# Kernel optimization log

Measured on AMD Instinct MI355X. Metric: run time of the kernel, lower is better.

Reference implementation:

```python
import jax, jax.numpy as jnp
import numpy as np

B, T, D, H = 64, 257, 1024, 16
F = 4096
R = 16
HD = D // H


def _layer_norm(x, g, b, eps=1e-5):
    mu = x.mean(-1, keepdims=True)
    var = x.var(-1, keepdims=True)
    return (x - mu) / jnp.sqrt(var + eps) * g + b


def _quick_gelu(x):
    return x * jax.nn.sigmoid(1.702 * x)


def _attention(x, Wq, bq, Wk, bk, Wv, bv, Wo, bo):
    scale = HD ** -0.5
    q = (x @ Wq + bq) * scale
    k = x @ Wk + bk
    v = x @ Wv + bv
    q = q.reshape(B, T, H, HD).transpose(0, 2, 1, 3)
    k = k.reshape(B, T, H, HD).transpose(0, 2, 1, 3)
    v = v.reshape(B, T, H, HD).transpose(0, 2, 1, 3)
    attn = jax.nn.softmax(jnp.einsum('bhqd,bhkd->bhqk', q, k), axis=-1)
    o = jnp.einsum('bhqk,bhkd->bhqd', attn, v)
    o = o.transpose(0, 2, 1, 3).reshape(B, T, D)
    return o @ Wo + bo


def _match_indices(metric, r, class_token=True):
    # cosine-normalized bipartite matching (no-grad path in torch; index-only here)
    m = metric / jnp.linalg.norm(metric, axis=-1, keepdims=True)
    a, b = m[:, ::2, :], m[:, 1::2, :]        # [B, ta, D], [B, tb, D]
    scores = jnp.einsum('nac,nbc->nab', a, b)  # [B, ta, tb]
    if class_token:
        scores = scores.at[:, 0, :].set(-jnp.inf)
    node_max = scores.max(-1)
    node_idx = scores.argmax(-1)
    edge_idx = jnp.argsort(-node_max, axis=-1)  # descending
    unm_idx = edge_idx[:, r:]
    src_idx = edge_idx[:, :r]
    dst_idx = jnp.take_along_axis(node_idx, src_idx, axis=-1)
    if class_token:
        unm_idx = jnp.sort(unm_idx, axis=1)
    return unm_idx, src_idx, dst_idx


def _merge_sum(x, unm_idx, src_idx, dst_idx):
    src, dst = x[:, ::2, :], x[:, 1::2, :]
    c = x.shape[-1]
    unm = jnp.take_along_axis(src, unm_idx[..., None], axis=1)       # [B, ta-r, c]
    sel = jnp.take_along_axis(src, src_idx[..., None], axis=1)       # [B, r, c]
    dst = jax.vmap(lambda d, di, sv: d.at[di].add(sv))(dst, dst_idx, sel)
    return jnp.concatenate([unm, dst], axis=1)                       # [B, T-r, c]


def setup_inputs() -> dict:
    key = jax.random.key(0)
    ks = jax.random.split(key, 12)
    s = 0.02
    return {
        'hidden_states': jax.random.normal(ks[0], (B, T, D), jnp.float32),
        'ln1_g': jnp.ones((D,), jnp.float32),
        'ln1_b': jnp.zeros((D,), jnp.float32),
        'Wq': jax.random.normal(ks[1], (D, D), jnp.float32) * s,
        'bq': jnp.zeros((D,), jnp.float32),
        'Wk': jax.random.normal(ks[2], (D, D), jnp.float32) * s,
        'bk': jnp.zeros((D,), jnp.float32),
        'Wv': jax.random.normal(ks[3], (D, D), jnp.float32) * s,
        'bv': jnp.zeros((D,), jnp.float32),
        'Wo': jax.random.normal(ks[4], (D, D), jnp.float32) * s,
        'bo': jnp.zeros((D,), jnp.float32),
        'ln2_g': jnp.ones((D,), jnp.float32),
        'ln2_b': jnp.zeros((D,), jnp.float32),
        'W1': jax.random.normal(ks[5], (D, F), jnp.float32) * s,
        'b1': jnp.zeros((F,), jnp.float32),
        'W2': jax.random.normal(ks[6], (F, D), jnp.float32) * s,
        'b2': jnp.zeros((D,), jnp.float32),
    }


def reference(hidden_states, ln1_g, ln1_b, Wq, bq, Wk, bk, Wv, bv, Wo, bo,
              ln2_g, ln2_b, W1, b1, W2, b2):
    # 1) LN1 + self-attention + residual
    x = hidden_states + _attention(_layer_norm(hidden_states, ln1_g, ln1_b),
                                   Wq, bq, Wk, bk, Wv, bv, Wo, bo)
    # 2) ToMe merge with weighted average (initial size = ones -> merge_wavg)
    metric = jax.lax.stop_gradient(x)
    unm_idx, src_idx, dst_idx = _match_indices(metric, R, class_token=True)
    size = jnp.ones((B, T, 1), x.dtype)
    x = _merge_sum(x * size, unm_idx, src_idx, dst_idx)
    size = _merge_sum(size, unm_idx, src_idx, dst_idx)
    x = x / size
    # 3) LN2 + MLP (quick_gelu) + residual
    h = _layer_norm(x, ln2_g, ln2_b)
    h = _quick_gelu(h @ W1 + b1) @ W2 + b2
    return x + h  # [B, T - R, D]
```

## Files before the change

kernel.cpp:

```cpp
#include <hip/hip_runtime.h>
#include <math.h>

#define BB 64
#define TT 257
#define DD 1024
#define HH 16
#define FF 4096
#define RR 16
#define HDD 64
#define TMM 241
#define M1 (BB*TT)
#define M2 (BB*TMM)
#define NA 129
#define NB 128

typedef float f4v __attribute__((ext_vector_type(4)));
typedef short s8v __attribute__((ext_vector_type(8)));
typedef short s4v __attribute__((ext_vector_type(4)));
typedef unsigned short us;

__device__ __forceinline__ us f2bf(float f){
  unsigned u = __float_as_uint(f);
  u += 0x7fffu + ((u >> 16) & 1u);
  return (us)(u >> 16);
}
__device__ __forceinline__ float bf2f(us h){
  return __uint_as_float(((unsigned)h) << 16);
}
__device__ __forceinline__ void gl16(const us* g, us* l){
  __builtin_amdgcn_global_load_lds((const __attribute__((address_space(1))) void*)g,
                                   (__attribute__((address_space(3))) void*)l, 16, 0, 0);
}

__global__ __launch_bounds__(64) void lnstats_kernel(const float* __restrict__ x,
                                                     float* __restrict__ st)
{
  int row = blockIdx.x, lane = threadIdx.x;
  const float* p = x + (size_t)row * DD;
  float s = 0.0f, sq = 0.0f;
  #pragma unroll
  for (int i = 0; i < 4; i++){
    float4 v = *(const float4*)(p + i * 256 + lane * 4);
    s  += v.x + v.y + v.z + v.w;
    sq += v.x*v.x + v.y*v.y + v.z*v.z + v.w*v.w;
  }
  #pragma unroll
  for (int m = 1; m < 64; m <<= 1){ s += __shfl_xor(s, m); sq += __shfl_xor(sq, m); }
  if (lane == 0){
    float mu  = s * (1.0f / DD);
    float var = sq * (1.0f / DD) - mu * mu;
    st[2*row]     = mu;
    st[2*row + 1] = 1.0f / sqrtf(var + 1e-5f);
  }
}

__global__ __launch_bounds__(256) void lncvt_kernel(const float* __restrict__ x,
    const float* __restrict__ st, const float* __restrict__ g,
    const float* __restrict__ b, us* __restrict__ out)
{
  int row = blockIdx.x, tid = threadIdx.x;
  float mu = st[2*row], rstd = st[2*row + 1];
  float4 xv = *(const float4*)(x + (size_t)row * DD + tid * 4);
  float4 gv = *(const float4*)(g + tid * 4);
  float4 bv = *(const float4*)(b + tid * 4);
  s4v o;
  o[0] = (short)f2bf((xv.x - mu) * rstd * gv.x + bv.x);
  o[1] = (short)f2bf((xv.y - mu) * rstd * gv.y + bv.y);
  o[2] = (short)f2bf((xv.z - mu) * rstd * gv.z + bv.z);
  o[3] = (short)f2bf((xv.w - mu) * rstd * gv.w + bv.w);
  *(s4v*)(out + (size_t)row * DD + tid * 4) = o;
}

__global__ __launch_bounds__(256) void wt_kernel(const float* __restrict__ src,
                                                 us* __restrict__ dhi,
                                                 us* __restrict__ dlo,
                                                 const float* __restrict__ gscale,
                                                 int K, int N)
{
  __shared__ float t[32][33];
  int tx = threadIdx.x, ty = threadIdx.y;
  int n0 = blockIdx.x * 32, k0 = blockIdx.y * 32;
  #pragma unroll
  for (int r = 0; r < 4; r++)
    t[ty + 8*r][tx] = src[(size_t)(k0 + ty + 8*r) * N + n0 + tx];
  __syncthreads();
  float gs = gscale ? gscale[k0 + tx] : 1.0f;
  #pragma unroll
  for (int r = 0; r < 4; r++){
    float f = t[tx][ty + 8*r] * gs;
    us hi = f2bf(f);
    size_t o = (size_t)(n0 + ty + 8*r) * K + k0 + tx;
    dhi[o] = hi;
    if (dlo) dlo[o] = f2bf(f - bf2f(hi));
  }
}

__global__ __launch_bounds__(256) void qc_kernel(const float* __restrict__ Wq,
    const float* __restrict__ Wk, const float* __restrict__ Wv,
    const float* __restrict__ g, const float* __restrict__ b,
    float* __restrict__ c1, float* __restrict__ c2)
{
  __shared__ float p1[4][64], p2[4][64];
  int n0 = blockIdx.x * 64;
  int kind = n0 >> 10, col0 = n0 & 1023;
  const float* W = (kind == 0) ? Wq : (kind == 1) ? Wk : Wv;
  int tx = threadIdx.x & 63, ty = threadIdx.x >> 6;
  float s1 = 0.0f, s2 = 0.0f;
  for (int k = ty; k < 1024; k += 4){
    float w = W[(size_t)k * 1024 + col0 + tx];
    s1 += g[k] * w;
    s2 += b[k] * w;
  }
  p1[ty][tx] = s1; p2[ty][tx] = s2;
  __syncthreads();
  if (ty == 0){
    c1[n0 + tx] = p1[0][tx] + p1[1][tx] + p1[2][tx] + p1[3][tx];
    c2[n0 + tx] = p2[0][tx] + p2[1][tx] + p2[2][tx] + p2[3][tx];
  }
}

__global__ __launch_bounds__(256) void qkv_kernel(const float* __restrict__ hidden,
    const us* __restrict__ WBh, const us* __restrict__ WBl,
    const float* __restrict__ bq, const float* __restrict__ bk, const float* __restrict__ bv,
    const float* __restrict__ lnstat, const float* __restrict__ c1, const float* __restrict__ c2,
    us* __restrict__ qhp, us* __restrict__ qlp, us* __restrict__ khp,
    us* __restrict__ klp, us* __restrict__ vhp, us* __restrict__ vlp)
{
  const int M = M1, K = DD;
  __shared__ __align__(16) us Ah[128*32];
  __shared__ __align__(16) us Bh[128*32];
  __shared__ __align__(16) us Al[128*32];
  __shared__ __align__(16) us Bl[128*32];
  int tid = threadIdx.x;
  int m0 = blockIdx.y * 128, n0 = blockIdx.x * 128;
  int lane = tid & 63, w = tid >> 6;
  int wr = w >> 1, wc = w & 1;
  int fr = lane & 15, fq = lane >> 4;
  f4v acc[4][4];
  f4v zero = {0.0f, 0.0f, 0.0f, 0.0f};
  #pragma unroll
  for (int i = 0; i < 4; i++)
    #pragma unroll
    for (int j = 0; j < 4; j++) acc[i][j] = zero;
  int sr = tid >> 2, sc4 = (tid & 3) * 8;
  int ar0 = m0 + sr;       if (ar0 >= M) ar0 = M - 1;
  int ar1 = m0 + 64 + sr;  if (ar1 >= M) ar1 = M - 1;
  int lr = lane >> 2, lc = (lane & 3) * 8;
  int gb0 = n0 + w*32 + lr;

  for (int kk = 0; kk < K; kk += 32){
    #pragma unroll
    for (int half = 0; half < 2; half++){
      int ar = half ? ar1 : ar0;
      const float* ap = hidden + (size_t)ar * K + kk + sc4;
      float4 fa = *(const float4*)(ap);
      float4 fb = *(const float4*)(ap + 4);
      float fv[8] = {fa.x, fa.y, fa.z, fa.w, fb.x, fb.y, fb.z, fb.w};
      s8v h, l;
      #pragma unroll
      for (int j = 0; j < 8; j++){
        us hi = f2bf(fv[j]);
        h[j] = (short)hi;
        l[j] = (short)f2bf(fv[j] - bf2f(hi));
      }
      int lrow = half * 64 + sr;
      *(s8v*)&Ah[lrow*32 + sc4] = h;
      *(s8v*)&Al[lrow*32 + sc4] = l;
    }
    gl16(WBh + (size_t)gb0 * K + kk + lc,        &Bh[(w*32)*32]);
    gl16(WBh + (size_t)(gb0 + 16) * K + kk + lc, &Bh[(w*32 + 16)*32]);
    gl16(WBl + (size_t)gb0 * K + kk + lc,        &Bl[(w*32)*32]);
    gl16(WBl + (size_t)(gb0 + 16) * K + kk + lc, &Bl[(w*32 + 16)*32]);
    __syncthreads();
    s8v ah[4], bh[4], al[4], bl[4];
    #pragma unroll
    for (int m = 0; m < 4; m++){
      ah[m] = *(const s8v*)&Ah[(wr*64 + m*16 + fr)*32 + fq*8];
      al[m] = *(const s8v*)&Al[(wr*64 + m*16 + fr)*32 + fq*8];
    }
    #pragma unroll
    for (int n = 0; n < 4; n++){
      bh[n] = *(const s8v*)&Bh[(wc*64 + n*16 + fr)*32 + fq*8];
      bl[n] = *(const s8v*)&Bl[(wc*64 + n*16 + fr)*32 + fq*8];
    }
    #pragma unroll
    for (int m = 0; m < 4; m++)
      #pragma unroll
      for (int n = 0; n < 4; n++){
        acc[m][n] = __builtin_amdgcn_mfma_f32_16x16x32_bf16(ah[m], bh[n], acc[m][n], 0, 0, 0);
        acc[m][n] = __builtin_amdgcn_mfma_f32_16x16x32_bf16(ah[m], bl[n], acc[m][n], 0, 0, 0);
        acc[m][n] = __builtin_amdgcn_mfma_f32_16x16x32_bf16(al[m], bh[n], acc[m][n], 0, 0, 0);
      }
    __syncthreads();
  }
  int kind = n0 >> 10;
  const float* bsel = (kind == 0) ? bq : (kind == 1) ? bk : bv;
  us* C0 = (kind == 0) ? qhp : (kind == 1) ? khp : vhp;
  us* C1 = (kind == 0) ? qlp : (kind == 1) ? klp : vlp;
  float scl = (kind == 0) ? 0.125f : 1.0f;
  #pragma unroll
  for (int m = 0; m < 4; m++){
    int grow0 = m0 + wr*64 + m*16 + fq*4;
    #pragma unroll
    for (int n = 0; n < 4; n++){
      int gcol = n0 + wc*64 + n*16 + fr;
      int lcn = gcol & 1023;
      int h2 = lcn >> 6, d2 = lcn & 63;
      float cc1 = c1[gcol], cc2 = c2[gcol] + bsel[lcn];
      #pragma unroll
      for (int i = 0; i < 4; i++){
        int grow = grow0 + i;
        if (grow < M){
          float mu = lnstat[2*grow], rstd = lnstat[2*grow + 1];
          int b2 = grow / 257;
          int t2 = grow - b2 * 257;
          size_t off2 = ((size_t)(b2*16 + h2) * 257 + t2) * 64 + d2;
          float v = (rstd * acc[m][n][i] - rstd * mu * cc1 + cc2) * scl;
          us hi = f2bf(v);
          C0[off2] = hi;
          C1[off2] = f2bf(v - bf2f(hi));
        }
      }
    }
  }
}

template<int AMODE, int SPLIT, int EPI>
__global__ __launch_bounds__(256) void gemm2_kernel(const us* __restrict__ Ahp,
    const us* __restrict__ Alp,
    const us* __restrict__ BTh, const us* __restrict__ BTl,
    const float* __restrict__ bias, const float* __restrict__ resid,
    void* __restrict__ C0, int M, int N, int K)
{
  __shared__ __align__(16) us Ah[128*32];
  __shared__ __align__(16) us Bh[128*32];
  __shared__ __align__(16) us Al[SPLIT ? 128*32 : 8];
  __shared__ __align__(16) us Bl[SPLIT ? 128*32 : 8];
  int tid = threadIdx.x;
  int m0 = blockIdx.y * 128, n0 = blockIdx.x * 128;
  int lane = tid & 63, w = tid >> 6;
  int wr = w >> 1, wc = w & 1;
  int fr = lane & 15, fq = lane >> 4;
  f4v acc[4][4];
  f4v zero = {0.0f, 0.0f, 0.0f, 0.0f};
  #pragma unroll
  for (int i = 0; i < 4; i++)
    #pragma unroll
    for (int j = 0; j < 4; j++) acc[i][j] = zero;
  int lr = lane >> 2, lc = (lane & 3) * 8;
  int ga0 = m0 + w*32 + lr;      if (ga0 >= M) ga0 = M - 1;
  int ga1 = m0 + w*32 + 16 + lr; if (ga1 >= M) ga1 = M - 1;
  int gb0 = n0 + w*32 + lr;
  int b2a = ga0 / 257, t2a = ga0 - b2a * 257;
  int b2b = ga1 / 257, t2b = ga1 - b2b * 257;

  for (int kk = 0; kk < K; kk += 32){
    if (AMODE == 1){
      gl16(Ahp + (size_t)ga0 * K + kk + lc, &Ah[(w*32)*32]);
      gl16(Ahp + (size_t)ga1 * K + kk + lc, &Ah[(w*32 + 16)*32]);
      if (SPLIT){
        gl16(Alp + (size_t)ga0 * K + kk + lc, &Al[(w*32)*32]);
        gl16(Alp + (size_t)ga1 * K + kk + lc, &Al[(w*32 + 16)*32]);
      }
    } else {
      int h2 = kk >> 6, d2 = (kk & 63) + lc;
      size_t o0 = ((size_t)(b2a*16 + h2) * 257 + t2a) * 64 + d2;
      size_t o1 = ((size_t)(b2b*16 + h2) * 257 + t2b) * 64 + d2;
      gl16(Ahp + o0, &Ah[(w*32)*32]);
      gl16(Ahp + o1, &Ah[(w*32 + 16)*32]);
      if (SPLIT){
        gl16(Alp + o0, &Al[(w*32)*32]);
        gl16(Alp + o1, &Al[(w*32 + 16)*32]);
      }
    }
    gl16(BTh + (size_t)gb0 * K + kk + lc,        &Bh[(w*32)*32]);
    gl16(BTh + (size_t)(gb0 + 16) * K + kk + lc, &Bh[(w*32 + 16)*32]);
    if (SPLIT){
      gl16(BTl + (size_t)gb0 * K + kk + lc,        &Bl[(w*32)*32]);
      gl16(BTl + (size_t)(gb0 + 16) * K + kk + lc, &Bl[(w*32 + 16)*32]);
    }
    __syncthreads();
    s8v ah[4], bh[4], al[4], bl[4];
    #pragma unroll
    for (int m = 0; m < 4; m++){
      ah[m] = *(const s8v*)&Ah[(wr*64 + m*16 + fr)*32 + fq*8];
      if (SPLIT) al[m] = *(const s8v*)&Al[(wr*64 + m*16 + fr)*32 + fq*8];
    }
    #pragma unroll
    for (int n = 0; n < 4; n++){
      bh[n] = *(const s8v*)&Bh[(wc*64 + n*16 + fr)*32 + fq*8];
      if (SPLIT) bl[n] = *(const s8v*)&Bl[(wc*64 + n*16 + fr)*32 + fq*8];
    }
    #pragma unroll
    for (int m = 0; m < 4; m++)
      #pragma unroll
      for (int n = 0; n < 4; n++){
        acc[m][n] = __builtin_amdgcn_mfma_f32_16x16x32_bf16(ah[m], bh[n], acc[m][n], 0, 0, 0);
        if (SPLIT){
          acc[m][n] = __builtin_amdgcn_mfma_f32_16x16x32_bf16(ah[m], bl[n], acc[m][n], 0, 0, 0);
          acc[m][n] = __builtin_amdgcn_mfma_f32_16x16x32_bf16(al[m], bh[n], acc[m][n], 0, 0, 0);
        }
      }
    __syncthreads();
  }
  #pragma unroll
  for (int m = 0; m < 4; m++){
    int grow0 = m0 + wr*64 + m*16 + fq*4;
    #pragma unroll
    for (int n = 0; n < 4; n++){
      int gcol = n0 + wc*64 + n*16 + fr;
      float bcol = bias[gcol];
      #pragma unroll
      for (int i = 0; i < 4; i++){
        int grow = grow0 + i;
        if (grow < M){
          float v = acc[m][n][i] + bcol;
          size_t off = (size_t)grow * N + gcol;
          if (EPI == 1){
            ((float*)C0)[off] = v + resid[off];
          } else {
            float gq = v / (1.0f + expf(-1.702f * v));
            ((us*)C0)[off] = f2bf(gq);
          }
        }
      }
    }
  }
}

__global__ __launch_bounds__(512, 1) void attn_flash_kernel(
    const us* __restrict__ Qh, const us* __restrict__ Ql,
    const us* __restrict__ Kh, const us* __restrict__ Klo,
    const us* __restrict__ Vh, const us* __restrict__ Vlo,
    us* Oh, us* Ol)
{
  __shared__ __align__(16) us Kl[257 * 128];
  __shared__ __align__(16) us Vl[64 * 640];
  int bh = blockIdx.x;
  const size_t hb = (size_t)bh * 257 * 64;
  int tid = threadIdx.x;
  int l = tid & 63, w = tid >> 6;
  int g = l >> 4, c = l & 15;
  const float NEG = -3.0e38f;

  {
    s8v z8 = {0,0,0,0,0,0,0,0};
    for (int idx = tid; idx < 64*640/8; idx += 512)
      *((s8v*)Vl + idx) = z8;
  }
  __syncthreads();
  for (int idx = tid; idx < 257*8; idx += 512){
    int tok = idx >> 3, ch = idx & 7;
    int sw = (tok & 7) << 4;
    s8v hv = *(const s8v*)(Kh  + hb + (size_t)tok * 64 + ch*8);
    s8v lv = *(const s8v*)(Klo + hb + (size_t)tok * 64 + ch*8);
    char* kr = (char*)Kl + tok * 256;
    *(s8v*)(kr + ((ch*16) ^ sw)) = hv;
    *(s8v*)(kr + 128 + ((ch*16) ^ sw)) = lv;
  }
  for (int idx = tid; idx < 257*8; idx += 512){
    int tok = idx >> 3, ch = idx & 7;
    s8v hv = *(const s8v*)(Vh  + hb + (size_t)tok * 64 + ch*8);
    s8v lv = *(const s8v*)(Vlo + hb + (size_t)tok * 64 + ch*8);
    #pragma unroll
    for (int j = 0; j < 8; j++){
      int d = ch*8 + j;
      char* vr = (char*)Vl + d * 1280;
      int off = (tok * 2) ^ (j << 4);
      *(us*)(vr + off) = (us)hv[j];
      *(us*)(vr + 640 + off) = (us)lv[j];
    }
  }
  __syncthreads();

  for (int qt = w; qt < 17; qt += 8){
    int t0 = qt * 16;
    int qr = t0 + c; if (qr > 256) qr = 256;
    const us* qp  = Qh + hb + (size_t)qr * 64 + g*8;
    const us* qp2 = Ql + hb + (size_t)qr * 64 + g*8;
    s8v qhi[2], qlo[2];
    qhi[0] = *(const s8v*)(qp);       qhi[1] = *(const s8v*)(qp + 32);
    qlo[0] = *(const s8v*)(qp2);      qlo[1] = *(const s8v*)(qp2 + 32);

    float m_run = NEG, l_run = 0.0f;
    f4v o4[4];
    #pragma unroll
    for (int dt = 0; dt < 4; dt++) o4[dt] = (f4v){0.0f, 0.0f, 0.0f, 0.0f};

    #pragma unroll 1
    for (int mck = 0; mck < 9; mck++){
      f4v a0, a1;
      {
        int t = 2*mck;
        int krow = t * 16 + c; if (krow > 256) krow = 256;
        char* kr = (char*)Kl + krow * 256;
        int sw = (krow & 7) << 4;
        s8v khi0 = *(const s8v*)(kr + ((g * 16) ^ sw));
        s8v khi1 = *(const s8v*)(kr + ((64 + g * 16) ^ sw));
        s8v klo0 = *(const s8v*)(kr + 128 + ((g * 16) ^ sw));
        s8v klo1 = *(const s8v*)(kr + 128 + ((64 + g * 16) ^ sw));
        f4v a = {0.0f, 0.0f, 0.0f, 0.0f};
        a = __builtin_amdgcn_mfma_f32_16x16x32_bf16(khi0, qhi[0], a, 0, 0, 0);
        a = __builtin_amdgcn_mfma_f32_16x16x32_bf16(khi1, qhi[1], a, 0, 0, 0);
        a = __builtin_amdgcn_mfma_f32_16x16x32_bf16(khi0, qlo[0], a, 0, 0, 0);
        a = __builtin_amdgcn_mfma_f32_16x16x32_bf16(khi1, qlo[1], a, 0, 0, 0);
        a = __builtin_amdgcn_mfma_f32_16x16x32_bf16(klo0, qhi[0], a, 0, 0, 0);
        a = __builtin_amdgcn_mfma_f32_16x16x32_bf16(klo1, qhi[1], a, 0, 0, 0);
        a0 = a;
      }
      if (mck < 8){
        int t = 2*mck + 1;
        int krow = t * 16 + c; if (krow > 256) krow = 256;
        char* kr = (char*)Kl + krow * 256;
        int sw = (krow & 7) << 4;
        s8v khi0 = *(const s8v*)(kr + ((g * 16) ^ sw));
        s8v khi1 = *(const s8v*)(kr + ((64 + g * 16) ^ sw));
        s8v klo0 = *(const s8v*)(kr + 128 + ((g * 16) ^ sw));
        s8v klo1 = *(const s8v*)(kr + 128 + ((64 + g * 16) ^ sw));
        f4v a = {0.0f, 0.0f, 0.0f, 0.0f};
        a = __builtin_amdgcn_mfma_f32_16x16x32_bf16(khi0, qhi[0], a, 0, 0, 0);
        a = __builtin_amdgcn_mfma_f32_16x16x32_bf16(khi1, qhi[1], a, 0, 0, 0);
        a = __builtin_amdgcn_mfma_f32_16x16x32_bf16(khi0, qlo[0], a, 0, 0, 0);
        a = __builtin_amdgcn_mfma_f32_16x16x32_bf16(khi1, qlo[1], a, 0, 0, 0);
        a = __builtin_amdgcn_mfma_f32_16x16x32_bf16(klo0, qhi[0], a, 0, 0, 0);
        a = __builtin_amdgcn_mfma_f32_16x16x32_bf16(klo1, qhi[1], a, 0, 0, 0);
        a1 = a;
      } else {
        a1 = (f4v){NEG, NEG, NEG, NEG};
        a0[0] = (g == 0) ? a0[0] : NEG;
        a0[1] = NEG; a0[2] = NEG; a0[3] = NEG;
      }
      float cm = fmaxf(fmaxf(fmaxf(a0[0], a0[1]), fmaxf(a0[2], a0[3])),
                       fmaxf(fmaxf(a1[0], a1[1]), fmaxf(a1[2], a1[3])));
      cm = fmaxf(cm, __shfl_xor(cm, 16));
      cm = fmaxf(cm, __shfl_xor(cm, 32));
      float m_new = fmaxf(m_run, cm);
      float scl = __expf(m_run - m_new);
      m_run = m_new;
      l_run *= scl;
      #pragma unroll
      for (int dt = 0; dt < 4; dt++){
        o4[dt][0] *= scl; o4[dt][1] *= scl; o4[dt][2] *= scl; o4[dt][3] *= scl;
      }
      float ls = 0.0f;
      unsigned Ph2[2][2], Pl2[2][2];
      #pragma unroll
      for (int k2 = 0; k2 < 2; k2++){
        float e0 = __expf(a0[2*k2] - m_new), e1 = __expf(a0[2*k2+1] - m_new);
        ls += e0 + e1;
        us h0 = f2bf(e0), h1 = f2bf(e1);
        Ph2[0][k2] = (unsigned)h0 | ((unsigned)h1 << 16);
        Pl2[0][k2] = (unsigned)f2bf(e0 - bf2f(h0)) | ((unsigned)f2bf(e1 - bf2f(h1)) << 16);
        float e2 = __expf(a1[2*k2] - m_new), e3 = __expf(a1[2*k2+1] - m_new);
        ls += e2 + e3;
        us h2 = f2bf(e2), h3 = f2bf(e3);
        Ph2[1][k2] = (unsigned)h2 | ((unsigned)h3 << 16);
        Pl2[1][k2] = (unsigned)f2bf(e2 - bf2f(h2)) | ((unsigned)f2bf(e3 - bf2f(h3)) << 16);
      }
      l_run += ls;
      s8v pbh, pbl;
      #pragma unroll
      for (int ww = 0; ww < 4; ww++){
        int srcl = (((g & 1) * 2 + (ww >> 1)) << 4) | c;
        unsigned h0 = (unsigned)__shfl((int)Ph2[0][ww & 1], srcl, 64);
        unsigned lo0 = (unsigned)__shfl((int)Pl2[0][ww & 1], srcl, 64);
        unsigned h1 = (unsigned)__shfl((int)Ph2[1][ww & 1], srcl, 64);
        unsigned lo1 = (unsigned)__shfl((int)Pl2[1][ww & 1], srcl, 64);
        ((unsigned*)&pbh)[ww] = (g >> 1) ? h1 : h0;
        ((unsigned*)&pbl)[ww] = (g >> 1) ? lo1 : lo0;
      }
      #pragma unroll
      for (int dt = 0; dt < 4; dt++){
        int d = dt * 16 + c;
        char* vr = (char*)Vl + d * 1280;
        int off = (mck * 64 + g * 16) ^ ((d & 7) << 4);
        s8v vh = *(const s8v*)(vr + off);
        s8v vlo = *(const s8v*)(vr + 640 + off);
        o4[dt] = __builtin_amdgcn_mfma_f32_16x16x32_bf16(vh, pbh, o4[dt], 0, 0, 0);
        o4[dt] = __builtin_amdgcn_mfma_f32_16x16x32_bf16(vh, pbl, o4[dt], 0, 0, 0);
        o4[dt] = __builtin_amdgcn_mfma_f32_16x16x32_bf16(vlo, pbh, o4[dt], 0, 0, 0);
      }
    }
    l_run += __shfl_xor(l_run, 16);
    l_run += __shfl_xor(l_run, 32);
    float inv = 1.0f / l_run;
    int qrow = t0 + c;
    if (qrow <= 256){
      us* oph = Oh + hb + (size_t)qrow * 64;
      us* opl = Ol + hb + (size_t)qrow * 64;
      #pragma unroll
      for (int dt = 0; dt < 4; dt++){
        s4v hv4, lv4;
        #pragma unroll
        for (int i = 0; i < 4; i++){
          float ov = o4[dt][i] * inv;
          us hi = f2bf(ov);
          hv4[i] = (short)hi;
          lv4[i] = (short)f2bf(ov - bf2f(hi));
        }
        *(s4v*)(oph + dt*16 + g*4) = hv4;
        *(s4v*)(opl + dt*16 + g*4) = lv4;
      }
    }
  }
}

__global__ __launch_bounds__(64) void norms_kernel(const float* __restrict__ x, float* __restrict__ nrm)
{
  int row = blockIdx.x, lane = threadIdx.x;
  const float* p = x + (size_t)row * DD;
  float sq = 0.0f;
  #pragma unroll
  for (int i = 0; i < 4; i++){
    float4 v = *(const float4*)(p + i * 256 + lane * 4);
    sq += v.x*v.x + v.y*v.y + v.z*v.z + v.w*v.w;
  }
  #pragma unroll
  for (int m = 1; m < 64; m <<= 1) sq += __shfl_xor(sq, m);
  if (lane == 0) nrm[row] = sqrtf(sq);
}

__global__ __launch_bounds__(256) void scores_kernel(const float* __restrict__ x,
                                                     const float* __restrict__ nrm,
                                                     float* __restrict__ sc)
{
  __shared__ __align__(16) float as_[16][1028];
  __shared__ __align__(16) float bs_[16][1028];
  int it = blockIdx.x, b = blockIdx.y;
  int tid = threadIdx.x;
  int rloc = tid >> 4, chunk = tid & 15;
  {
    int i = it * 16 + rloc;
    int tg = (i < NA) ? 2 * i : 2 * (NA - 1);
    const float* p = x + ((size_t)b * TT + tg) * DD + chunk * 64;
    #pragma unroll
    for (int ii = 0; ii < 16; ii++)
      *(float4*)&as_[rloc][chunk * 64 + 4*ii] = *(const float4*)(p + 4*ii);
  }
  for (int jt = 0; jt < 8; jt++){
    __syncthreads();
    {
      int j = jt * 16 + rloc;
      const float* p = x + ((size_t)b * TT + 2*j + 1) * DD + chunk * 64;
      #pragma unroll
      for (int ii = 0; ii < 16; ii++)
        *(float4*)&bs_[rloc][chunk * 64 + 4*ii] = *(const float4*)(p + 4*ii);
    }
    __syncthreads();
    int iloc = tid >> 4, jloc = tid & 15;
    float sum = 0.0f;
    #pragma unroll 8
    for (int cgg = 0; cgg < 1024; cgg += 4){
      float4 av = *(const float4*)&as_[iloc][cgg];
      float4 bvv = *(const float4*)&bs_[jloc][cgg];
      sum += av.x*bvv.x + av.y*bvv.y + av.z*bvv.z + av.w*bvv.w;
    }
    int i = it * 16 + iloc, j = jt * 16 + jloc;
    if (i < NA){
      float val = sum / (nrm[(size_t)b * TT + 2*i] * nrm[(size_t)b * TT + 2*j + 1]);
      sc[((size_t)b * NA + i) * NB + j] = val;
    }
  }
}

__global__ __launch_bounds__(64) void node_kernel(const float* __restrict__ sc,
                                                  float* __restrict__ nmax, int* __restrict__ nidx)
{
  int i = blockIdx.x, b = blockIdx.y, lane = threadIdx.x;
  const float* row = sc + ((size_t)b * NA + i) * NB;
  float v0 = row[lane];
  float v1 = row[lane + 64];
  float bv = v0; int bi = lane;
  if (v1 > bv){ bv = v1; bi = lane + 64; }
  #pragma unroll
  for (int m = 1; m < 64; m <<= 1){
    float ov = __shfl_xor(bv, m);
    int oi = __shfl_xor(bi, m);
    if (ov > bv || (ov == bv && oi < bi)){ bv = ov; bi = oi; }
  }
  if (lane == 0){
    if (i == 0){ nmax[(size_t)b * NA] = -INFINITY; nidx[(size_t)b * NA] = 0; }
    else { nmax[(size_t)b * NA + i] = bv; nidx[(size_t)b * NA + i] = bi; }
  }
}

__global__ __launch_bounds__(256) void rank_kernel(const float* __restrict__ nmax,
    const int* __restrict__ nidx, int* __restrict__ src, int* __restrict__ dst,
    int* __restrict__ unm, int* __restrict__ cnt)
{
  __shared__ float v[NA];
  __shared__ int rk[NA];
  __shared__ int edge[NA];
  __shared__ int cs[NB];
  int b = blockIdx.x, t = threadIdx.x;
  if (t < NA) v[t] = nmax[(size_t)b * NA + t];
  if (t < NB) cs[t] = 0;
  __syncthreads();
  if (t < NA){
    float vt = v[t]; int r = 0;
    for (int i = 0; i < NA; i++){
      float vi = v[i];
      r += (vi > vt) || (vi == vt && i < t);
    }
    rk[t] = r; edge[r] = t;
  }
  __syncthreads();
  if (t < RR){
    int s = edge[t];
    src[b * RR + t] = s;
    int d = nidx[(size_t)b * NA + s];
    dst[b * RR + t] = d;
    atomicAdd(&cs[d], 1);
  }
  if (t < NA && rk[t] >= RR){
    int p = 0;
    for (int i = 0; i < NA; i++) p += (i < t) && (rk[i] >= RR);
    unm[b * (NA - RR) + p] = t;
  }
  __syncthreads();
  if (t < NB) cnt[b * NB + t] = cs[t];
}

__global__ __launch_bounds__(256) void merge_kernel(const float* __restrict__ x,
    const int* __restrict__ src, const int* __restrict__ dst, const int* __restrict__ unm,
    const int* __restrict__ cnt, float* __restrict__ xm)
{
  int u = blockIdx.x, b = blockIdx.y;
  int c = threadIdx.x * 4;
  const float* xb = x + (size_t)b * TT * DD;
  float4 acc;
  if (u < NA - RR){
    int ts = 2 * unm[b * (NA - RR) + u];
    acc = *(const float4*)(xb + (size_t)ts * DD + c);
  } else {
    int j = u - (NA - RR);
    acc = *(const float4*)(xb + (size_t)(2*j + 1) * DD + c);
    #pragma unroll
    for (int k2 = 0; k2 < RR; k2++){
      if (dst[b * RR + k2] == j){
        int ts = 2 * src[b * RR + k2];
        float4 av = *(const float4*)(xb + (size_t)ts * DD + c);
        acc.x += av.x; acc.y += av.y; acc.z += av.z; acc.w += av.w;
      }
    }
    float inv = 1.0f / (float)(1 + cnt[b * NB + j]);
    acc.x *= inv; acc.y *= inv; acc.z *= inv; acc.w *= inv;
  }
  *(float4*)(xm + ((size_t)b * TMM + u) * DD + c) = acc;
}

extern "C" void kernel_launch(void* const* d_in, const int* in_sizes, int n_in,
                              void* d_out, int out_size, void* d_ws, size_t ws_size,
                              hipStream_t stream)
{
  (void)in_sizes; (void)n_in; (void)out_size; (void)ws_size;
  const float* hidden = (const float*)d_in[0];
  const float* ln1_g  = (const float*)d_in[1];
  const float* ln1_b  = (const float*)d_in[2];
  const float* Wq = (const float*)d_in[3];
  const float* bq = (const float*)d_in[4];
  const float* Wk = (const float*)d_in[5];
  const float* bk = (const float*)d_in[6];
  const float* Wv = (const float*)d_in[7];
  const float* bv = (const float*)d_in[8];
  const float* Wo = (const float*)d_in[9];
  const float* bo = (const float*)d_in[10];
  const float* ln2_g = (const float*)d_in[11];
  const float* ln2_b = (const float*)d_in[12];
  const float* W1 = (const float*)d_in[13];
  const float* b1 = (const float*)d_in[14];
  const float* W2 = (const float*)d_in[15];
  const float* b2 = (const float*)d_in[16];

  char* base = (char*)d_ws;
  const size_t PE = (size_t)M1 * DD;
  const size_t PL = PE * sizeof(us);
  us* qh = (us*)base;          us* ql = qh + PE;
  us* kh = (us*)(base + 2*PL); us* kl = kh + PE;
  us* vh = (us*)(base + 4*PL); us* vl = vh + PE;
  us* wts = (us*)(base + 6*PL);
  const size_t WD = (size_t)DD * DD;
  us* wqh = wts;
  us* wkh = wqh + WD;
  us* wvh = wkh + WD;
  us* wql = wvh + WD;
  us* wkl = wql + WD;
  us* wvl = wkl + WD;
  us* woh = wvl + WD;
  us* wol = woh + WD;
  us* w1h = wol + WD;
  us* w2h = w1h + (size_t)DD * FF;
  float* lnst1 = (float*)(w2h + (size_t)FF * DD);
  float* c1p   = lnst1 + 2 * M1;
  float* c2p   = c1p + 3072;
  float* xb = (float*)(base + 2*PL);
  float* nrm   = (float*)(base + 4*PL);
  float* sc    = nrm + M1;
  float* nmaxp = sc + (size_t)BB * NA * NB;
  int*   nidxp = (int*)(nmaxp + BB * NA);
  int*   srcI  = nidxp + BB * NA;
  int*   dstI  = srcI + BB * RR;
  int*   unmI  = dstI + BB * RR;
  int*   cntI  = unmI + BB * (NA - RR);
  us*    xh2   = (us*)(base + 4*PL + (size_t)8*1024*1024);
  float* lnst2 = (float*)(base + 4*PL + (size_t)48*1024*1024);
  float* xm = (float*)d_out;
  us* mid = (us*)base;

  dim3 tb32(32, 8);
  wt_kernel<<<dim3(DD/32, DD/32), tb32, 0, stream>>>(Wq, wqh, wql, ln1_g, DD, DD);
  wt_kernel<<<dim3(DD/32, DD/32), tb32, 0, stream>>>(Wk, wkh, wkl, ln1_g, DD, DD);
  wt_kernel<<<dim3(DD/32, DD/32), tb32, 0, stream>>>(Wv, wvh, wvl, ln1_g, DD, DD);
  wt_kernel<<<dim3(DD/32, DD/32), tb32, 0, stream>>>(Wo, woh, wol, nullptr, DD, DD);
  wt_kernel<<<dim3(FF/32, DD/32), tb32, 0, stream>>>(W1, w1h, nullptr, nullptr, DD, FF);
  wt_kernel<<<dim3(DD/32, FF/32), tb32, 0, stream>>>(W2, w2h, nullptr, nullptr, FF, DD);

  qc_kernel<<<48, 256, 0, stream>>>(Wq, Wk, Wv, ln1_g, ln1_b, c1p, c2p);
  lnstats_kernel<<<M1, 64, 0, stream>>>(hidden, lnst1);

  qkv_kernel<<<dim3(3072/128, (M1 + 127)/128), 256, 0, stream>>>(hidden, wqh, wql,
      bq, bk, bv, lnst1, c1p, c2p, qh, ql, kh, kl, vh, vl);

  attn_flash_kernel<<<BB*HH, 512, 0, stream>>>(qh, ql, kh, kl, vh, vl, qh, ql);

  gemm2_kernel<2,1,1><<<dim3(DD/128, (M1 + 127)/128), 256, 0, stream>>>(qh, ql, woh, wol,
      bo, hidden, xb, M1, DD, DD);

  norms_kernel<<<M1, 64, 0, stream>>>(xb, nrm);
  scores_kernel<<<dim3(9, BB), 256, 0, stream>>>(xb, nrm, sc);
  node_kernel<<<dim3(NA, BB), 64, 0, stream>>>(sc, nmaxp, nidxp);
  rank_kernel<<<BB, 256, 0, stream>>>(nmaxp, nidxp, srcI, dstI, unmI, cntI);
  merge_kernel<<<dim3(TMM, BB), 256, 0, stream>>>(xb, srcI, dstI, unmI, cntI, xm);

  lnstats_kernel<<<M2, 64, 0, stream>>>(xm, lnst2);
  lncvt_kernel<<<M2, 256, 0, stream>>>(xm, lnst2, ln2_g, ln2_b, xh2);

  gemm2_kernel<1,0,2><<<dim3(FF/128, (M2 + 127)/128), 256, 0, stream>>>(xh2, nullptr, w1h, nullptr,
      b1, nullptr, mid, M2, FF, DD);
  gemm2_kernel<1,0,1><<<dim3(DD/128, (M2 + 127)/128), 256, 0, stream>>>(mid, nullptr, w2h, nullptr,
      b2, xm, (float*)d_out, M2, DD, FF);
}
```

Measured before the change: 1.724 ms.

## Widen QKV GEMM tile to 128x256 with 512 threads and cheaper bf16 split

```diff
diff --git a/kernel.cpp b/kernel.cpp
--- a/kernel.cpp
+++ b/kernel.cpp
@@ -27,6 +27,14 @@
 __device__ __forceinline__ float bf2f(us h){
   return __uint_as_float(((unsigned)h) << 16);
 }
+__device__ __forceinline__ void splitpk(float f0, float f1, unsigned &hp, unsigned &lp){
+  unsigned u0 = __float_as_uint(f0), u1 = __float_as_uint(f1);
+  unsigned h0m = u0 & 0xFFFF0000u, h1m = u1 & 0xFFFF0000u;
+  hp = (u0 >> 16) | h1m;
+  float l0 = f0 - __uint_as_float(h0m);
+  float l1 = f1 - __uint_as_float(h1m);
+  lp = (__float_as_uint(l0) >> 16) | (__float_as_uint(l1) & 0xFFFF0000u);
+}
 __device__ __forceinline__ void gl16(const us* g, us* l){
   __builtin_amdgcn_global_load_lds((const __attribute__((address_space(1))) void*)g,
                                    (__attribute__((address_space(3))) void*)l, 16, 0, 0);
@@ -119,7 +127,7 @@
   }
 }
 
-__global__ __launch_bounds__(256) void qkv_kernel(const float* __restrict__ hidden,
+__global__ __launch_bounds__(512) void qkv_kernel(const float* __restrict__ hidden,
     const us* __restrict__ WBh, const us* __restrict__ WBl,
     const float* __restrict__ bq, const float* __restrict__ bk, const float* __restrict__ bv,
     const float* __restrict__ lnstat, const float* __restrict__ c1, const float* __restrict__ c2,
@@ -127,14 +135,14 @@
     us* __restrict__ klp, us* __restrict__ vhp, us* __restrict__ vlp)
 {
   const int M = M1, K = DD;
-  __shared__ __align__(16) us Ah[128*32];
-  __shared__ __align__(16) us Bh[128*32];
-  __shared__ __align__(16) us Al[128*32];
-  __shared__ __align__(16) us Bl[128*32];
+  __shared__ __align__(16) us Ah[128*40];
+  __shared__ __align__(16) us Al[128*40];
+  __shared__ __align__(16) us Bh[256*32];
+  __shared__ __align__(16) us Bl[256*32];
   int tid = threadIdx.x;
-  int m0 = blockIdx.y * 128, n0 = blockIdx.x * 128;
+  int m0 = blockIdx.y * 128, n0 = blockIdx.x * 256;
   int lane = tid & 63, w = tid >> 6;
-  int wr = w >> 1, wc = w & 1;
+  int wr = w >> 2, wc = w & 3;
   int fr = lane & 15, fq = lane >> 4;
   f4v acc[4][4];
   f4v zero = {0.0f, 0.0f, 0.0f, 0.0f};
@@ -143,29 +151,24 @@
     #pragma unroll
     for (int j = 0; j < 4; j++) acc[i][j] = zero;
   int sr = tid >> 2, sc4 = (tid & 3) * 8;
-  int ar0 = m0 + sr;       if (ar0 >= M) ar0 = M - 1;
-  int ar1 = m0 + 64 + sr;  if (ar1 >= M) ar1 = M - 1;
+  int ar = m0 + sr; if (ar >= M) ar = M - 1;
   int lr = lane >> 2, lc = (lane & 3) * 8;
   int gb0 = n0 + w*32 + lr;
 
   for (int kk = 0; kk < K; kk += 32){
-    #pragma unroll
-    for (int half = 0; half < 2; half++){
-      int ar = half ? ar1 : ar0;
+    {
       const float* ap = hidden + (size_t)ar * K + kk + sc4;
       float4 fa = *(const float4*)(ap);
       float4 fb = *(const float4*)(ap + 4);
-      float fv[8] = {fa.x, fa.y, fa.z, fa.w, fb.x, fb.y, fb.z, fb.w};
-      s8v h, l;
-      #pragma unroll
-      for (int j = 0; j < 8; j++){
-        us hi = f2bf(fv[j]);
-        h[j] = (short)hi;
-        l[j] = (short)f2bf(fv[j] - bf2f(hi));
-      }
-      int lrow = half * 64 + sr;
-      *(s8v*)&Ah[lrow*32 + sc4] = h;
-      *(s8v*)&Al[lrow*32 + sc4] = l;
+      unsigned h0, h1, h2, h3, l0, l1, l2, l3;
+      splitpk(fa.x, fa.y, h0, l0);
+      splitpk(fa.z, fa.w, h1, l1);
+      splitpk(fb.x, fb.y, h2, l2);
+      splitpk(fb.z, fb.w, h3, l3);
+      uint4 hv = {h0, h1, h2, h3};
+      uint4 lv = {l0, l1, l2, l3};
+      *(uint4*)&Ah[sr*40 + sc4] = hv;
+      *(uint4*)&Al[sr*40 + sc4] = lv;
     }
     gl16(WBh + (size_t)gb0 * K + kk + lc,        &Bh[(w*32)*32]);
     gl16(WBh + (size_t)(gb0 + 16) * K + kk + lc, &Bh[(w*32 + 16)*32]);
@@ -175,8 +178,8 @@
     s8v ah[4], bh[4], al[4], bl[4];
     #pragma unroll
     for (int m = 0; m < 4; m++){
-      ah[m] = *(const s8v*)&Ah[(wr*64 + m*16 + fr)*32 + fq*8];
-      al[m] = *(const s8v*)&Al[(wr*64 + m*16 + fr)*32 + fq*8];
+      ah[m] = *(const s8v*)&Ah[(wr*64 + m*16 + fr)*40 + fq*8];
+      al[m] = *(const s8v*)&Al[(wr*64 + m*16 + fr)*40 + fq*8];
     }
     #pragma unroll
     for (int n = 0; n < 4; n++){
@@ -195,30 +198,36 @@
   }
   int kind = n0 >> 10;
   const float* bsel = (kind == 0) ? bq : (kind == 1) ? bk : bv;
-  us* C0 = (kind == 0) ? qhp : (kind == 1) ? khp : vhp;
-  us* C1 = (kind == 0) ? qlp : (kind == 1) ? klp : vlp;
+  us* O0 = (kind == 0) ? qhp : (kind == 1) ? khp : vhp;
+  us* O1 = (kind == 0) ? qlp : (kind == 1) ? klp : vlp;
   float scl = (kind == 0) ? 0.125f : 1.0f;
+  float C1r[4], C2r[4];
+  int h2r[4], d2r[4];
+  #pragma unroll
+  for (int n = 0; n < 4; n++){
+    int gcol = n0 + wc*64 + n*16 + fr;
+    int lcn = gcol & 1023;
+    h2r[n] = lcn >> 6; d2r[n] = lcn & 63;
+    C1r[n] = c1[gcol];
+    C2r[n] = c2[gcol] + bsel[lcn];
+  }
   #pragma unroll
   for (int m = 0; m < 4; m++){
     int grow0 = m0 + wr*64 + m*16 + fq*4;
     #pragma unroll
-    for (int n = 0; n < 4; n++){
-      int gcol = n0 + wc*64 + n*16 + fr;
-      int lcn = gcol & 1023;
-      int h2 = lcn >> 6, d2 = lcn & 63;
-      float cc1 = c1[gcol], cc2 = c2[gcol] + bsel[lcn];
-      #pragma unroll
-      for (int i = 0; i < 4; i++){
-        int grow = grow0 + i;
-        if (grow < M){
-          float mu = lnstat[2*grow], rstd = lnstat[2*grow + 1];
-          int b2 = grow / 257;
-          int t2 = grow - b2 * 257;
-          size_t off2 = ((size_t)(b2*16 + h2) * 257 + t2) * 64 + d2;
-          float v = (rstd * acc[m][n][i] - rstd * mu * cc1 + cc2) * scl;
+    for (int i = 0; i < 4; i++){
+      int grow = grow0 + i;
+      if (grow < M){
+        float mu = lnstat[2*grow], rstd = lnstat[2*grow + 1];
+        int b2 = grow / 257, t2 = grow - b2 * 257;
+        size_t rb = ((size_t)(b2*16) * 257 + t2) * 64;
+        #pragma unroll
+        for (int n = 0; n < 4; n++){
+          size_t off2 = rb + (size_t)h2r[n] * (257*64) + d2r[n];
+          float v = (rstd * acc[m][n][i] - rstd * mu * C1r[n] + C2r[n]) * scl;
           us hi = f2bf(v);
-          C0[off2] = hi;
-          C1[off2] = f2bf(v - bf2f(hi));
+          O0[off2] = hi;
+          O1[off2] = f2bf(v - bf2f(hi));
         }
       }
     }
@@ -718,7 +727,7 @@
   qc_kernel<<<48, 256, 0, stream>>>(Wq, Wk, Wv, ln1_g, ln1_b, c1p, c2p);
   lnstats_kernel<<<M1, 64, 0, stream>>>(hidden, lnst1);
 
-  qkv_kernel<<<dim3(3072/128, (M1 + 127)/128), 256, 0, stream>>>(hidden, wqh, wql,
+  qkv_kernel<<<dim3(3072/256, (M1 + 127)/128), 512, 0, stream>>>(hidden, wqh, wql,
       bq, bk, bv, lnst1, c1p, c2p, qh, ql, kh, kl, vh, vl);
 
   attn_flash_kernel<<<BB*HH, 512, 0, stream>>>(qh, ql, kh, kl, vh, vl, qh, ql);
```

Measured after the change: 1.584 ms. 8.1% less time.
